# Performance work log

Measured on AMD Instinct MI355X. Metric: run time of the kernel, lower is better.

The kernel has to match this reference:

```python
import jax, jax.numpy as jnp
import numpy as np

N_HEADS = 4
D_K = 64


def setup_inputs() -> dict:
    key = jax.random.key(0)
    k1, k2, k3, k4, k5 = jax.random.split(key, 5)
    C = 256
    return {
        "x": jax.random.normal(k1, (16, C, 32, 32), dtype=jnp.float32),
        "W_qkv": jax.random.normal(k2, (C, N_HEADS * D_K * 3), dtype=jnp.float32) * (C ** -0.5),
        "b_qkv": jax.random.normal(k3, (N_HEADS * D_K * 3,), dtype=jnp.float32) * 0.02,
        "W_out": jax.random.normal(k4, (N_HEADS * D_K, C), dtype=jnp.float32) * ((N_HEADS * D_K) ** -0.5),
        "b_out": jax.random.normal(k5, (C,), dtype=jnp.float32) * 0.02,
    }


def reference(x, W_qkv, b_qkv, W_out, b_out):
    # NOTE: the original forward never applies self.norm and ignores t.
    B, C, H, W = x.shape
    N = H * W
    scale = D_K ** -0.5
    xf = x.reshape(B, C, N).transpose(0, 2, 1)            # [B, N, C]
    qkv = (xf @ W_qkv + b_qkv).reshape(B, N, N_HEADS, 3 * D_K)
    q, k, v = jnp.split(qkv, 3, axis=-1)                  # each [B, N, H, dk]
    attn = jnp.einsum('bihd,bjhd->bijh', q, k) * scale    # [B, N, N, H]
    attn = jax.nn.softmax(attn, axis=2)                   # softmax over keys (j)
    res = jnp.einsum('bijh,bjhd->bihd', attn, v)          # [B, N, H, dk]
    res = res.reshape(B, N, N_HEADS * D_K)
    res = res @ W_out + b_out + xf                        # residual on flattened x
    return res.transpose(0, 2, 1).reshape(B, C, H, W)
```

## Files before the change

kernel.cpp:

```cpp
#include <hip/hip_runtime.h>
#include <math.h>

#define NN 1024

typedef __attribute__((ext_vector_type(8))) __bf16 bf16x8;
typedef __attribute__((ext_vector_type(4))) float f32x4;

__device__ __forceinline__ unsigned short f2bf(float f) {
    unsigned u = __float_as_uint(f);
    unsigned r = (u + 0x7fff + ((u >> 16) & 1)) >> 16;
    return (unsigned short)r;
}

__global__ __launch_bounds__(256) void prep_transpose(
    const float* __restrict__ x, const float* __restrict__ Wq,
    const float* __restrict__ Wo,
    unsigned short* __restrict__ xb, unsigned short* __restrict__ Wqt,
    unsigned short* __restrict__ Wot)
{
    __shared__ __align__(16) unsigned short T[64 * 72];
    const int bx = blockIdx.x;
    const int rt = blockIdx.y;
    const float* src; unsigned short* dst; int ncol, c0;
    if (bx < 256) {
        int b = bx >> 4; int ct = bx & 15;
        src = x + (size_t)b * 256 * 1024; dst = xb + (size_t)b * 1024 * 256;
        ncol = 1024; c0 = ct * 64;
    } else if (bx < 268) {
        src = Wq; dst = Wqt; ncol = 768; c0 = (bx - 256) * 64;
    } else {
        src = Wo; dst = Wot; ncol = 256; c0 = (bx - 268) * 64;
    }
    const int t = threadIdx.x;
    #pragma unroll
    for (int i = 0; i < 4; ++i) {
        int r  = i * 16 + (t >> 4);
        int c4 = (t & 15) * 4;
        float4 v = *(const float4*)&src[(size_t)(rt * 64 + r) * ncol + c0 + c4];
        ushort4 u; u.x = f2bf(v.x); u.y = f2bf(v.y); u.z = f2bf(v.z); u.w = f2bf(v.w);
        *(ushort4*)&T[r * 72 + c4] = u;
    }
    __syncthreads();
    #pragma unroll
    for (int i = 0; i < 2; ++i) {
        int task = t + 256 * i;
        int c = task & 63, rs = task >> 6;
        ushort u8[8];
        #pragma unroll
        for (int k = 0; k < 8; ++k) u8[k] = T[(rs * 8 + k) * 72 + c];
        *(uint4*)&dst[(size_t)(c0 + c) * 256 + rt * 64 + rs * 8] = *(uint4*)u8;
    }
}

__global__ __launch_bounds__(256, 4) void qkv_gemm(
    const unsigned short* __restrict__ xb, const unsigned short* __restrict__ Wqt,
    const float* __restrict__ bias,
    unsigned short* __restrict__ Qb, unsigned short* __restrict__ Kb,
    unsigned short* __restrict__ Vtb)
{
    __shared__ __align__(16) unsigned short As[128 * 40];
    __shared__ __align__(16) unsigned short Bs[128 * 40];
    const int jt = blockIdx.x;
    const int m0 = blockIdx.y * 128;
    const int b  = m0 >> 10;
    const int n0 = m0 & 1023;
    const int t = threadIdx.x;
    const int w = t >> 6, lane = t & 63, quad = lane >> 4, cc = lane & 15;
    const int wm = (w & 1) * 64;
    const int wj = (w >> 1) * 64;

    f32x4 acc[4][4];
    #pragma unroll
    for (int ms = 0; ms < 4; ++ms)
        #pragma unroll
        for (int js = 0; js < 4; ++js) acc[ms][js] = (f32x4)(0.f);

    for (int k0 = 0; k0 < 256; k0 += 32) {
        __syncthreads();
        #pragma unroll
        for (int i = 0; i < 2; ++i) {
            int flat = t + 256 * i;
            int row = flat >> 2, seg = flat & 3;
            *(uint4*)&As[row * 40 + seg * 8] =
                *(const uint4*)&xb[(size_t)(m0 + row) * 256 + k0 + seg * 8];
            *(uint4*)&Bs[row * 40 + seg * 8] =
                *(const uint4*)&Wqt[(size_t)(jt * 128 + row) * 256 + k0 + seg * 8];
        }
        __syncthreads();
        bf16x8 af[4], bfr[4];
        #pragma unroll
        for (int ms = 0; ms < 4; ++ms)
            af[ms] = *(bf16x8*)&As[(wm + ms * 16 + cc) * 40 + quad * 8];
        #pragma unroll
        for (int js = 0; js < 4; ++js)
            bfr[js] = *(bf16x8*)&Bs[(wj + js * 16 + cc) * 40 + quad * 8];
        #pragma unroll
        for (int ms = 0; ms < 4; ++ms)
            #pragma unroll
            for (int js = 0; js < 4; ++js)
                acc[ms][js] = __builtin_amdgcn_mfma_f32_16x16x32_bf16(
                    af[ms], bfr[js], acc[ms][js], 0, 0, 0);
    }

    const int chunk = jt * 2 + (w >> 1);
    const int h = chunk / 3, type = chunk % 3;
    const size_t bh = (size_t)b * 4 + h;
    float bias_r[4];
    #pragma unroll
    for (int js = 0; js < 4; ++js) bias_r[js] = bias[jt * 128 + wj + js * 16 + cc];

    if (type == 2) {
        #pragma unroll
        for (int ms = 0; ms < 4; ++ms)
            #pragma unroll
            for (int js = 0; js < 4; ++js) {
                int dd = js * 16 + cc;
                int n = n0 + wm + ms * 16 + quad * 4;
                ushort4 u;
                u.x = f2bf(acc[ms][js][0] + bias_r[js]);
                u.y = f2bf(acc[ms][js][1] + bias_r[js]);
                u.z = f2bf(acc[ms][js][2] + bias_r[js]);
                u.w = f2bf(acc[ms][js][3] + bias_r[js]);
                *(ushort4*)&Vtb[(bh * 64 + dd) * NN + n] = u;
            }
    } else {
        unsigned short* dst = type ? Kb : Qb;
        const float sc = type ? 1.0f : 0.125f;
        #pragma unroll
        for (int ms = 0; ms < 4; ++ms)
            #pragma unroll
            for (int js = 0; js < 4; ++js)
                #pragma unroll
                for (int r = 0; r < 4; ++r) {
                    int n = n0 + wm + ms * 16 + quad * 4 + r;
                    dst[(bh * NN + n) * 64 + js * 16 + cc] =
                        f2bf((acc[ms][js][r] + bias_r[js]) * sc);
                }
    }
}

__global__ __launch_bounds__(256, 4) void flash_attn(
    const unsigned short* __restrict__ Qb, const unsigned short* __restrict__ Kb,
    const unsigned short* __restrict__ Vtb, unsigned short* __restrict__ resb)
{
    __shared__ __align__(16) unsigned short Qs[64 * 72];
    __shared__ __align__(16) unsigned short Ks[64 * 72];
    __shared__ __align__(16) unsigned short Vt[64 * 72];
    __shared__ __align__(16) unsigned short Ps[64 * 72];

    const int blk = blockIdx.x;
    const int qt = blk & 15;
    const int h  = (blk >> 4) & 3;
    const int b  = blk >> 6;
    const int t  = threadIdx.x;
    const int w  = t >> 6;
    const int lane = t & 63;
    const int quad = lane >> 4;
    const int c    = lane & 15;

    const size_t bh = (size_t)(b * 4 + h);
    const unsigned short* Qg = Qb  + bh * NN * 64;
    const unsigned short* Kg = Kb  + bh * NN * 64;
    const unsigned short* Vg = Vtb + bh * 64 * NN;

    #pragma unroll
    for (int i = 0; i < 2; ++i) {
        int flat = t + 256 * i;
        int row = flat >> 3, seg = flat & 7;
        *(uint4*)&Qs[row * 72 + seg * 8] =
            *(const uint4*)&Qg[(size_t)(qt * 64 + row) * 64 + seg * 8];
    }

    float m_i = -INFINITY, l_i = 0.f;
    f32x4 O[4];
    #pragma unroll
    for (int dt = 0; dt < 4; ++dt) O[dt] = (f32x4)(0.f);

    for (int kt = 0; kt < 16; ++kt) {
        __syncthreads();
        #pragma unroll
        for (int i = 0; i < 2; ++i) {
            int flat = t + 256 * i;
            int row = flat >> 3, seg = flat & 7;
            *(uint4*)&Ks[row * 72 + seg * 8] =
                *(const uint4*)&Kg[(size_t)(kt * 64 + row) * 64 + seg * 8];
            *(uint4*)&Vt[row * 72 + seg * 8] =
                *(const uint4*)&Vg[(size_t)row * NN + kt * 64 + seg * 8];
        }
        __syncthreads();

        f32x4 S[4];
        #pragma unroll
        for (int jt = 0; jt < 4; ++jt) S[jt] = (f32x4)(0.f);
        #pragma unroll
        for (int ks = 0; ks < 2; ++ks) {
            bf16x8 qf = *(bf16x8*)&Qs[(w * 16 + c) * 72 + ks * 32 + quad * 8];
            #pragma unroll
            for (int jt = 0; jt < 4; ++jt) {
                bf16x8 kf = *(bf16x8*)&Ks[(jt * 16 + c) * 72 + ks * 32 + quad * 8];
                S[jt] = __builtin_amdgcn_mfma_f32_16x16x32_bf16(kf, qf, S[jt], 0, 0, 0);
            }
        }

        float mt = -INFINITY;
        #pragma unroll
        for (int jt = 0; jt < 4; ++jt)
            #pragma unroll
            for (int r = 0; r < 4; ++r) mt = fmaxf(mt, S[jt][r]);
        mt = fmaxf(mt, __shfl_xor(mt, 16));
        mt = fmaxf(mt, __shfl_xor(mt, 32));
        float mn = fmaxf(m_i, mt);
        float alpha = __expf(m_i - mn);
        float p[4][4];
        float rs = 0.f;
        #pragma unroll
        for (int jt = 0; jt < 4; ++jt)
            #pragma unroll
            for (int r = 0; r < 4; ++r) {
                p[jt][r] = __expf(S[jt][r] - mn);
                rs += p[jt][r];
            }
        rs += __shfl_xor(rs, 16);
        rs += __shfl_xor(rs, 32);
        l_i = l_i * alpha + rs;
        m_i = mn;

        #pragma unroll
        for (int jt = 0; jt < 4; ++jt) {
            ushort4 pv;
            pv.x = f2bf(p[jt][0]); pv.y = f2bf(p[jt][1]);
            pv.z = f2bf(p[jt][2]); pv.w = f2bf(p[jt][3]);
            *(ushort4*)&Ps[(w * 16 + c) * 72 + jt * 16 + quad * 4] = pv;
        }

        float alpha_r[4];
        #pragma unroll
        for (int r = 0; r < 4; ++r) alpha_r[r] = __shfl(alpha, quad * 4 + r);
        #pragma unroll
        for (int dt = 0; dt < 4; ++dt)
            #pragma unroll
            for (int r = 0; r < 4; ++r) O[dt][r] *= alpha_r[r];

        #pragma unroll
        for (int js = 0; js < 2; ++js) {
            bf16x8 pf = *(bf16x8*)&Ps[(w * 16 + c) * 72 + js * 32 + quad * 8];
            #pragma unroll
            for (int dt = 0; dt < 4; ++dt) {
                bf16x8 vf = *(bf16x8*)&Vt[(dt * 16 + c) * 72 + js * 32 + quad * 8];
                O[dt] = __builtin_amdgcn_mfma_f32_16x16x32_bf16(pf, vf, O[dt], 0, 0, 0);
            }
        }
    }

    float linv[4];
    #pragma unroll
    for (int r = 0; r < 4; ++r) linv[r] = 1.f / __shfl(l_i, quad * 4 + r);
    #pragma unroll
    for (int dt = 0; dt < 4; ++dt)
        #pragma unroll
        for (int r = 0; r < 4; ++r) {
            int row = qt * 64 + w * 16 + quad * 4 + r;
            resb[((size_t)(b * NN + row)) * 256 + h * 64 + dt * 16 + c] =
                f2bf(O[dt][r] * linv[r]);
        }
}

__global__ __launch_bounds__(256, 4) void out_gemm(
    const unsigned short* __restrict__ resb, const unsigned short* __restrict__ Wot,
    const float* __restrict__ bias, const float* __restrict__ x,
    float* __restrict__ out)
{
    __shared__ __align__(16) unsigned short As[64 * 40];
    __shared__ __align__(16) unsigned short Bs[64 * 40];
    const int n0 = blockIdx.x * 64;
    const int c0 = blockIdx.y * 64;
    const int b  = blockIdx.z;
    const int t = threadIdx.x;
    const int w = t >> 6, lane = t & 63, quad = lane >> 4, cc = lane & 15;
    const int wm = (w & 1) * 32;
    const int wj = (w >> 1) * 32;

    f32x4 acc[2][2];
    #pragma unroll
    for (int ms = 0; ms < 2; ++ms)
        #pragma unroll
        for (int js = 0; js < 2; ++js) acc[ms][js] = (f32x4)(0.f);

    for (int k0 = 0; k0 < 256; k0 += 32) {
        __syncthreads();
        {
            int r = t >> 2, seg = t & 3;
            *(uint4*)&As[r * 40 + seg * 8] =
                *(const uint4*)&resb[((size_t)b * NN + n0 + r) * 256 + k0 + seg * 8];
            *(uint4*)&Bs[r * 40 + seg * 8] =
                *(const uint4*)&Wot[(size_t)(c0 + r) * 256 + k0 + seg * 8];
        }
        __syncthreads();
        bf16x8 af[2], bfr[2];
        #pragma unroll
        for (int ms = 0; ms < 2; ++ms)
            af[ms] = *(bf16x8*)&As[(wm + ms * 16 + cc) * 40 + quad * 8];
        #pragma unroll
        for (int js = 0; js < 2; ++js)
            bfr[js] = *(bf16x8*)&Bs[(wj + js * 16 + cc) * 40 + quad * 8];
        #pragma unroll
        for (int ms = 0; ms < 2; ++ms)
            #pragma unroll
            for (int js = 0; js < 2; ++js)
                acc[ms][js] = __builtin_amdgcn_mfma_f32_16x16x32_bf16(
                    af[ms], bfr[js], acc[ms][js], 0, 0, 0);
    }

    #pragma unroll
    for (int js = 0; js < 2; ++js) {
        int c = c0 + wj + js * 16 + cc;
        float bi = bias[c];
        #pragma unroll
        for (int ms = 0; ms < 2; ++ms) {
            int n = n0 + wm + ms * 16 + quad * 4;
            size_t off = ((size_t)b * 256 + c) * NN + n;
            float4 xr = *(const float4*)&x[off];
            float4 o;
            o.x = acc[ms][js][0] + bi + xr.x;
            o.y = acc[ms][js][1] + bi + xr.y;
            o.z = acc[ms][js][2] + bi + xr.z;
            o.w = acc[ms][js][3] + bi + xr.w;
            *(float4*)&out[off] = o;
        }
    }
}

extern "C" void kernel_launch(void* const* d_in, const int* in_sizes, int n_in,
                              void* d_out, int out_size, void* d_ws, size_t ws_size,
                              hipStream_t stream)
{
    const float* x     = (const float*)d_in[0];
    const float* W_qkv = (const float*)d_in[1];
    const float* b_qkv = (const float*)d_in[2];
    const float* W_out = (const float*)d_in[3];
    const float* b_out = (const float*)d_in[4];
    float* out = (float*)d_out;

    char* wsc = (char*)d_ws;
    unsigned short* xb   = (unsigned short*)(wsc);
    unsigned short* Wqt  = (unsigned short*)(wsc + ((size_t)8 << 20));
    unsigned short* Wot  = (unsigned short*)(wsc + ((size_t)8 << 20) + ((size_t)512 << 10));
    unsigned short* Qb   = (unsigned short*)(wsc + ((size_t)9  << 20));
    unsigned short* Kb   = (unsigned short*)(wsc + ((size_t)17 << 20));
    unsigned short* Vtb  = (unsigned short*)(wsc + ((size_t)25 << 20));
    unsigned short* resb = (unsigned short*)(wsc + ((size_t)33 << 20));

    prep_transpose<<<dim3(272, 4), 256, 0, stream>>>(x, W_qkv, W_out, xb, Wqt, Wot);
    qkv_gemm<<<dim3(6, 128), 256, 0, stream>>>(xb, Wqt, b_qkv, Qb, Kb, Vtb);
    flash_attn<<<dim3(1024), 256, 0, stream>>>(Qb, Kb, Vtb, resb);
    out_gemm<<<dim3(16, 4, 16), 256, 0, stream>>>(resb, Wot, b_out, x, out);
}
```

Before: 147.6 us.

## Register-prefetch next tiles in GEMM and attention loops, use native bf16 conversion

```diff
diff --git a/kernel.cpp b/kernel.cpp
--- a/kernel.cpp
+++ b/kernel.cpp
@@ -4,12 +4,17 @@
 #define NN 1024
 
 typedef __attribute__((ext_vector_type(8))) __bf16 bf16x8;
+typedef __attribute__((ext_vector_type(4))) __bf16 bf16x4;
 typedef __attribute__((ext_vector_type(4))) float f32x4;
 
 __device__ __forceinline__ unsigned short f2bf(float f) {
-    unsigned u = __float_as_uint(f);
-    unsigned r = (u + 0x7fff + ((u >> 16) & 1)) >> 16;
-    return (unsigned short)r;
+    __bf16 h = (__bf16)f;
+    return *(unsigned short*)&h;
+}
+__device__ __forceinline__ ushort4 pack4(float a, float b, float c, float d) {
+    bf16x4 v;
+    v[0] = (__bf16)a; v[1] = (__bf16)b; v[2] = (__bf16)c; v[3] = (__bf16)d;
+    return *(ushort4*)&v;
 }
 
 __global__ __launch_bounds__(256) void prep_transpose(
@@ -37,8 +42,7 @@
         int r  = i * 16 + (t >> 4);
         int c4 = (t & 15) * 4;
         float4 v = *(const float4*)&src[(size_t)(rt * 64 + r) * ncol + c0 + c4];
-        ushort4 u; u.x = f2bf(v.x); u.y = f2bf(v.y); u.z = f2bf(v.z); u.w = f2bf(v.w);
-        *(ushort4*)&T[r * 72 + c4] = u;
+        *(ushort4*)&T[r * 72 + c4] = pack4(v.x, v.y, v.z, v.w);
     }
     __syncthreads();
     #pragma unroll
@@ -75,18 +79,33 @@
         #pragma unroll
         for (int js = 0; js < 4; ++js) acc[ms][js] = (f32x4)(0.f);
 
-    for (int k0 = 0; k0 < 256; k0 += 32) {
+    uint4 areg[2], breg[2];
+    #pragma unroll
+    for (int i = 0; i < 2; ++i) {
+        int flat = t + 256 * i;
+        int row = flat >> 2, seg = flat & 3;
+        areg[i] = *(const uint4*)&xb[(size_t)(m0 + row) * 256 + seg * 8];
+        breg[i] = *(const uint4*)&Wqt[(size_t)(jt * 128 + row) * 256 + seg * 8];
+    }
+
+    for (int kk = 0; kk < 8; ++kk) {
         __syncthreads();
         #pragma unroll
         for (int i = 0; i < 2; ++i) {
             int flat = t + 256 * i;
             int row = flat >> 2, seg = flat & 3;
-            *(uint4*)&As[row * 40 + seg * 8] =
-                *(const uint4*)&xb[(size_t)(m0 + row) * 256 + k0 + seg * 8];
-            *(uint4*)&Bs[row * 40 + seg * 8] =
-                *(const uint4*)&Wqt[(size_t)(jt * 128 + row) * 256 + k0 + seg * 8];
-        }
-        __syncthreads();
+            *(uint4*)&As[row * 40 + seg * 8] = areg[i];
+            *(uint4*)&Bs[row * 40 + seg * 8] = breg[i];
+        }
+        __syncthreads();
+        int kn = ((kk + 1) & 7) * 32;
+        #pragma unroll
+        for (int i = 0; i < 2; ++i) {
+            int flat = t + 256 * i;
+            int row = flat >> 2, seg = flat & 3;
+            areg[i] = *(const uint4*)&xb[(size_t)(m0 + row) * 256 + kn + seg * 8];
+            breg[i] = *(const uint4*)&Wqt[(size_t)(jt * 128 + row) * 256 + kn + seg * 8];
+        }
         bf16x8 af[4], bfr[4];
         #pragma unroll
         for (int ms = 0; ms < 4; ++ms)
@@ -116,12 +135,9 @@
             for (int js = 0; js < 4; ++js) {
                 int dd = js * 16 + cc;
                 int n = n0 + wm + ms * 16 + quad * 4;
-                ushort4 u;
-                u.x = f2bf(acc[ms][js][0] + bias_r[js]);
-                u.y = f2bf(acc[ms][js][1] + bias_r[js]);
-                u.z = f2bf(acc[ms][js][2] + bias_r[js]);
-                u.w = f2bf(acc[ms][js][3] + bias_r[js]);
-                *(ushort4*)&Vtb[(bh * 64 + dd) * NN + n] = u;
+                *(ushort4*)&Vtb[(bh * 64 + dd) * NN + n] =
+                    pack4(acc[ms][js][0] + bias_r[js], acc[ms][js][1] + bias_r[js],
+                          acc[ms][js][2] + bias_r[js], acc[ms][js][3] + bias_r[js]);
             }
     } else {
         unsigned short* dst = type ? Kb : Qb;
@@ -163,13 +179,20 @@
     const unsigned short* Kg = Kb  + bh * NN * 64;
     const unsigned short* Vg = Vtb + bh * 64 * NN;
 
+    uint4 kreg[2], vreg[2];
     #pragma unroll
     for (int i = 0; i < 2; ++i) {
         int flat = t + 256 * i;
         int row = flat >> 3, seg = flat & 7;
         *(uint4*)&Qs[row * 72 + seg * 8] =
             *(const uint4*)&Qg[(size_t)(qt * 64 + row) * 64 + seg * 8];
-    }
+        kreg[i] = *(const uint4*)&Kg[(size_t)row * 64 + seg * 8];
+        vreg[i] = *(const uint4*)&Vg[(size_t)row * NN + seg * 8];
+    }
+    __syncthreads();
+    bf16x8 qf[2];
+    qf[0] = *(bf16x8*)&Qs[(w * 16 + c) * 72 + 0 * 32 + quad * 8];
+    qf[1] = *(bf16x8*)&Qs[(w * 16 + c) * 72 + 1 * 32 + quad * 8];
 
     float m_i = -INFINITY, l_i = 0.f;
     f32x4 O[4];
@@ -182,23 +205,28 @@
         for (int i = 0; i < 2; ++i) {
             int flat = t + 256 * i;
             int row = flat >> 3, seg = flat & 7;
-            *(uint4*)&Ks[row * 72 + seg * 8] =
-                *(const uint4*)&Kg[(size_t)(kt * 64 + row) * 64 + seg * 8];
-            *(uint4*)&Vt[row * 72 + seg * 8] =
-                *(const uint4*)&Vg[(size_t)row * NN + kt * 64 + seg * 8];
-        }
-        __syncthreads();
+            *(uint4*)&Ks[row * 72 + seg * 8] = kreg[i];
+            *(uint4*)&Vt[row * 72 + seg * 8] = vreg[i];
+        }
+        __syncthreads();
+        int ktn = (kt + 1) & 15;
+        #pragma unroll
+        for (int i = 0; i < 2; ++i) {
+            int flat = t + 256 * i;
+            int row = flat >> 3, seg = flat & 7;
+            kreg[i] = *(const uint4*)&Kg[(size_t)(ktn * 64 + row) * 64 + seg * 8];
+            vreg[i] = *(const uint4*)&Vg[(size_t)row * NN + ktn * 64 + seg * 8];
+        }
 
         f32x4 S[4];
         #pragma unroll
         for (int jt = 0; jt < 4; ++jt) S[jt] = (f32x4)(0.f);
         #pragma unroll
         for (int ks = 0; ks < 2; ++ks) {
-            bf16x8 qf = *(bf16x8*)&Qs[(w * 16 + c) * 72 + ks * 32 + quad * 8];
             #pragma unroll
             for (int jt = 0; jt < 4; ++jt) {
                 bf16x8 kf = *(bf16x8*)&Ks[(jt * 16 + c) * 72 + ks * 32 + quad * 8];
-                S[jt] = __builtin_amdgcn_mfma_f32_16x16x32_bf16(kf, qf, S[jt], 0, 0, 0);
+                S[jt] = __builtin_amdgcn_mfma_f32_16x16x32_bf16(kf, qf[ks], S[jt], 0, 0, 0);
             }
         }
 
@@ -226,12 +254,9 @@
         m_i = mn;
 
         #pragma unroll
-        for (int jt = 0; jt < 4; ++jt) {
-            ushort4 pv;
-            pv.x = f2bf(p[jt][0]); pv.y = f2bf(p[jt][1]);
-            pv.z = f2bf(p[jt][2]); pv.w = f2bf(p[jt][3]);
-            *(ushort4*)&Ps[(w * 16 + c) * 72 + jt * 16 + quad * 4] = pv;
-        }
+        for (int jt = 0; jt < 4; ++jt)
+            *(ushort4*)&Ps[(w * 16 + c) * 72 + jt * 16 + quad * 4] =
+                pack4(p[jt][0], p[jt][1], p[jt][2], p[jt][3]);
 
         float alpha_r[4];
         #pragma unroll
@@ -279,6 +304,7 @@
     const int w = t >> 6, lane = t & 63, quad = lane >> 4, cc = lane & 15;
     const int wm = (w & 1) * 32;
     const int wj = (w >> 1) * 32;
+    const int r = t >> 2, seg = t & 3;
 
     f32x4 acc[2][2];
     #pragma unroll
@@ -286,16 +312,17 @@
         #pragma unroll
         for (int js = 0; js < 2; ++js) acc[ms][js] = (f32x4)(0.f);
 
-    for (int k0 = 0; k0 < 256; k0 += 32) {
-        __syncthreads();
-        {
-            int r = t >> 2, seg = t & 3;
-            *(uint4*)&As[r * 40 + seg * 8] =
-                *(const uint4*)&resb[((size_t)b * NN + n0 + r) * 256 + k0 + seg * 8];
-            *(uint4*)&Bs[r * 40 + seg * 8] =
-                *(const uint4*)&Wot[(size_t)(c0 + r) * 256 + k0 + seg * 8];
-        }
-        __syncthreads();
+    uint4 areg = *(const uint4*)&resb[((size_t)b * NN + n0 + r) * 256 + seg * 8];
+    uint4 breg = *(const uint4*)&Wot[(size_t)(c0 + r) * 256 + seg * 8];
+
+    for (int kk = 0; kk < 8; ++kk) {
+        __syncthreads();
+        *(uint4*)&As[r * 40 + seg * 8] = areg;
+        *(uint4*)&Bs[r * 40 + seg * 8] = breg;
+        __syncthreads();
+        int kn = ((kk + 1) & 7) * 32;
+        areg = *(const uint4*)&resb[((size_t)b * NN + n0 + r) * 256 + kn + seg * 8];
+        breg = *(const uint4*)&Wot[(size_t)(c0 + r) * 256 + kn + seg * 8];
         bf16x8 af[2], bfr[2];
         #pragma unroll
         for (int ms = 0; ms < 2; ++ms)
@@ -313,12 +340,12 @@
 
     #pragma unroll
     for (int js = 0; js < 2; ++js) {
-        int c = c0 + wj + js * 16 + cc;
-        float bi = bias[c];
+        int cI = c0 + wj + js * 16 + cc;
+        float bi = bias[cI];
         #pragma unroll
         for (int ms = 0; ms < 2; ++ms) {
             int n = n0 + wm + ms * 16 + quad * 4;
-            size_t off = ((size_t)b * 256 + c) * NN + n;
+            size_t off = ((size_t)b * 256 + cI) * NN + n;
             float4 xr = *(const float4*)&x[off];
             float4 o;
             o.x = acc[ms][js][0] + bi + xr.x;
```

Measured after the change: 208.6 us. +41.4%, slower.

## Double-buffer K/V tiles in flash attention with async global-to-LDS copies

Applied to the files above, without the earlier changes.

```diff
diff --git a/kernel.cpp b/kernel.cpp
--- a/kernel.cpp
+++ b/kernel.cpp
@@ -4,12 +4,24 @@
 #define NN 1024
 
 typedef __attribute__((ext_vector_type(8))) __bf16 bf16x8;
+typedef __attribute__((ext_vector_type(4))) __bf16 bf16x4;
 typedef __attribute__((ext_vector_type(4))) float f32x4;
 
 __device__ __forceinline__ unsigned short f2bf(float f) {
-    unsigned u = __float_as_uint(f);
-    unsigned r = (u + 0x7fff + ((u >> 16) & 1)) >> 16;
-    return (unsigned short)r;
+    __bf16 h = (__bf16)f;
+    return *(unsigned short*)&h;
+}
+__device__ __forceinline__ ushort4 pack4(float a, float b, float c, float d) {
+    bf16x4 v;
+    v[0] = (__bf16)a; v[1] = (__bf16)b; v[2] = (__bf16)c; v[3] = (__bf16)d;
+    return *(ushort4*)&v;
+}
+
+__device__ __forceinline__ void async_cp16(const unsigned short* g, unsigned short* l) {
+    __builtin_amdgcn_global_load_lds(
+        (const __attribute__((address_space(1))) unsigned int*)g,
+        (__attribute__((address_space(3))) unsigned int*)l,
+        16, 0, 0);
 }
 
 __global__ __launch_bounds__(256) void prep_transpose(
@@ -37,8 +49,7 @@
         int r  = i * 16 + (t >> 4);
         int c4 = (t & 15) * 4;
         float4 v = *(const float4*)&src[(size_t)(rt * 64 + r) * ncol + c0 + c4];
-        ushort4 u; u.x = f2bf(v.x); u.y = f2bf(v.y); u.z = f2bf(v.z); u.w = f2bf(v.w);
-        *(ushort4*)&T[r * 72 + c4] = u;
+        *(ushort4*)&T[r * 72 + c4] = pack4(v.x, v.y, v.z, v.w);
     }
     __syncthreads();
     #pragma unroll
@@ -116,12 +127,9 @@
             for (int js = 0; js < 4; ++js) {
                 int dd = js * 16 + cc;
                 int n = n0 + wm + ms * 16 + quad * 4;
-                ushort4 u;
-                u.x = f2bf(acc[ms][js][0] + bias_r[js]);
-                u.y = f2bf(acc[ms][js][1] + bias_r[js]);
-                u.z = f2bf(acc[ms][js][2] + bias_r[js]);
-                u.w = f2bf(acc[ms][js][3] + bias_r[js]);
-                *(ushort4*)&Vtb[(bh * 64 + dd) * NN + n] = u;
+                *(ushort4*)&Vtb[(bh * 64 + dd) * NN + n] =
+                    pack4(acc[ms][js][0] + bias_r[js], acc[ms][js][1] + bias_r[js],
+                          acc[ms][js][2] + bias_r[js], acc[ms][js][3] + bias_r[js]);
             }
     } else {
         unsigned short* dst = type ? Kb : Qb;
@@ -139,13 +147,15 @@
     }
 }
 
-__global__ __launch_bounds__(256, 4) void flash_attn(
+__global__ __launch_bounds__(256) void flash_attn(
     const unsigned short* __restrict__ Qb, const unsigned short* __restrict__ Kb,
     const unsigned short* __restrict__ Vtb, unsigned short* __restrict__ resb)
 {
-    __shared__ __align__(16) unsigned short Qs[64 * 72];
-    __shared__ __align__(16) unsigned short Ks[64 * 72];
-    __shared__ __align__(16) unsigned short Vt[64 * 72];
+    __shared__ __align__(16) unsigned short Qs[4096];
+    __shared__ __align__(16) unsigned short Ks0[4096];
+    __shared__ __align__(16) unsigned short Ks1[4096];
+    __shared__ __align__(16) unsigned short Vt0[4096];
+    __shared__ __align__(16) unsigned short Vt1[4096];
     __shared__ __align__(16) unsigned short Ps[64 * 72];
 
     const int blk = blockIdx.x;
@@ -165,10 +175,20 @@
 
     #pragma unroll
     for (int i = 0; i < 2; ++i) {
-        int flat = t + 256 * i;
-        int row = flat >> 3, seg = flat & 7;
-        *(uint4*)&Qs[row * 72 + seg * 8] =
-            *(const uint4*)&Qg[(size_t)(qt * 64 + row) * 64 + seg * 8];
+        int f = i * 256 + t;
+        int row = f >> 3;
+        int gc  = (f & 7) ^ (row & 7);
+        async_cp16(&Qg[(size_t)(qt * 64 + row) * 64 + gc * 8], &Qs[f * 8]);
+        async_cp16(&Kg[(size_t)row * 64 + gc * 8], &Ks0[f * 8]);
+        async_cp16(&Vg[(size_t)row * NN + gc * 8], &Vt0[f * 8]);
+    }
+    __syncthreads();
+
+    bf16x8 qf[2];
+    #pragma unroll
+    for (int ks = 0; ks < 2; ++ks) {
+        int sc_ = (ks * 4 + quad) ^ (c & 7);
+        qf[ks] = *(bf16x8*)&Qs[((w * 16 + c) * 8 + sc_) * 8];
     }
 
     float m_i = -INFINITY, l_i = 0.f;
@@ -176,29 +196,32 @@
     #pragma unroll
     for (int dt = 0; dt < 4; ++dt) O[dt] = (f32x4)(0.f);
 
-    for (int kt = 0; kt < 16; ++kt) {
-        __syncthreads();
-        #pragma unroll
-        for (int i = 0; i < 2; ++i) {
-            int flat = t + 256 * i;
-            int row = flat >> 3, seg = flat & 7;
-            *(uint4*)&Ks[row * 72 + seg * 8] =
-                *(const uint4*)&Kg[(size_t)(kt * 64 + row) * 64 + seg * 8];
-            *(uint4*)&Vt[row * 72 + seg * 8] =
-                *(const uint4*)&Vg[(size_t)row * NN + kt * 64 + seg * 8];
-        }
-        __syncthreads();
+    auto step = [&](int kt, const unsigned short* curK, const unsigned short* curV,
+                    unsigned short* nxtK, unsigned short* nxtV,
+                    bool pref, bool bar) {
+        if (bar) __syncthreads();
+        if (pref) {
+            int ktn = kt + 1;
+            #pragma unroll
+            for (int i = 0; i < 2; ++i) {
+                int f = i * 256 + t;
+                int row = f >> 3;
+                int gc  = (f & 7) ^ (row & 7);
+                async_cp16(&Kg[(size_t)(ktn * 64 + row) * 64 + gc * 8], &nxtK[f * 8]);
+                async_cp16(&Vg[(size_t)row * NN + ktn * 64 + gc * 8], &nxtV[f * 8]);
+            }
+        }
 
         f32x4 S[4];
         #pragma unroll
         for (int jt = 0; jt < 4; ++jt) S[jt] = (f32x4)(0.f);
         #pragma unroll
         for (int ks = 0; ks < 2; ++ks) {
-            bf16x8 qf = *(bf16x8*)&Qs[(w * 16 + c) * 72 + ks * 32 + quad * 8];
             #pragma unroll
             for (int jt = 0; jt < 4; ++jt) {
-                bf16x8 kf = *(bf16x8*)&Ks[(jt * 16 + c) * 72 + ks * 32 + quad * 8];
-                S[jt] = __builtin_amdgcn_mfma_f32_16x16x32_bf16(kf, qf, S[jt], 0, 0, 0);
+                int sc_ = (ks * 4 + quad) ^ (c & 7);
+                bf16x8 kf = *(bf16x8*)&curK[((jt * 16 + c) * 8 + sc_) * 8];
+                S[jt] = __builtin_amdgcn_mfma_f32_16x16x32_bf16(kf, qf[ks], S[jt], 0, 0, 0);
             }
         }
 
@@ -226,12 +249,9 @@
         m_i = mn;
 
         #pragma unroll
-        for (int jt = 0; jt < 4; ++jt) {
-            ushort4 pv;
-            pv.x = f2bf(p[jt][0]); pv.y = f2bf(p[jt][1]);
-            pv.z = f2bf(p[jt][2]); pv.w = f2bf(p[jt][3]);
-            *(ushort4*)&Ps[(w * 16 + c) * 72 + jt * 16 + quad * 4] = pv;
-        }
+        for (int jt = 0; jt < 4; ++jt)
+            *(ushort4*)&Ps[(w * 16 + c) * 72 + jt * 16 + quad * 4] =
+                pack4(p[jt][0], p[jt][1], p[jt][2], p[jt][3]);
 
         float alpha_r[4];
         #pragma unroll
@@ -246,11 +266,20 @@
             bf16x8 pf = *(bf16x8*)&Ps[(w * 16 + c) * 72 + js * 32 + quad * 8];
             #pragma unroll
             for (int dt = 0; dt < 4; ++dt) {
-                bf16x8 vf = *(bf16x8*)&Vt[(dt * 16 + c) * 72 + js * 32 + quad * 8];
+                int sc_ = (js * 4 + quad) ^ (c & 7);
+                bf16x8 vf = *(bf16x8*)&curV[((dt * 16 + c) * 8 + sc_) * 8];
                 O[dt] = __builtin_amdgcn_mfma_f32_16x16x32_bf16(pf, vf, O[dt], 0, 0, 0);
             }
         }
-    }
+    };
+
+    step(0, Ks0, Vt0, Ks1, Vt1, true, false);
+    for (int kt2 = 0; kt2 < 7; ++kt2) {
+        int kt = 2 * kt2 + 1;
+        step(kt,     Ks1, Vt1, Ks0, Vt0, true, true);
+        step(kt + 1, Ks0, Vt0, Ks1, Vt1, true, true);
+    }
+    step(15, Ks1, Vt1, Ks0, Vt0, false, true);
 
     float linv[4];
     #pragma unroll
@@ -313,12 +342,12 @@
 
     #pragma unroll
     for (int js = 0; js < 2; ++js) {
-        int c = c0 + wj + js * 16 + cc;
-        float bi = bias[c];
+        int cI = c0 + wj + js * 16 + cc;
+        float bi = bias[cI];
         #pragma unroll
         for (int ms = 0; ms < 2; ++ms) {
             int n = n0 + wm + ms * 16 + quad * 4;
-            size_t off = ((size_t)b * 256 + c) * NN + n;
+            size_t off = ((size_t)b * 256 + cI) * NN + n;
             float4 xr = *(const float4*)&x[off];
             float4 o;
             o.x = acc[ms][js][0] + bi + xr.x;
```

Measured after the change: 146.9 us. No clear change (-0.4%).
